# Kernel tuning notes

Hardware: AMD Instinct MI355X
Metric: run time of the kernel (lower is better)

## Reference

```python
import math
import jax, jax.numpy as jnp
import numpy as np

BS, NTOK, NHEADS, WIDTH, WIN = 2, 4096, 8, 32, 32


def _make_coo():
    d = np.repeat(np.arange(NTOK), WIN)
    j = np.tile(np.arange(WIN), NTOK)
    s = (d + j) % NTOK
    # dst_cnt = j (dense per-dst counter), src_cnt = j (dense per-src counter,
    # since for fixed src the contributing dsts have distinct j)
    return jnp.asarray(np.stack([d, s, j, j], axis=1), dtype=jnp.int32)


def setup_inputs() -> dict:
    key = jax.random.key(0)
    k1, k2, k3, k4 = jax.random.split(key, 4)
    shape = (BS, NTOK, NHEADS, WIDTH)
    return {
        "vf": jax.random.normal(k1, shape, dtype=jnp.float32),
        "vb": jax.random.normal(k2, shape, dtype=jnp.float32),
        "q": jax.random.normal(k3, shape, dtype=jnp.float32),
        "k": jax.random.normal(k4, shape, dtype=jnp.float32),
        "coo": _make_coo(),
        "dst_mxlen": WIN,
        "src_mxlen": WIN,
        "use_softmax": 1,
    }


def reference(vf, vb, q, k, coo, dst_mxlen, src_mxlen, use_softmax):
    # q,k,vf,vb: [bs, n_tok, n_heads, width]; coo: [cl,4] = [dst,src,dst_cnt,src_cnt]
    # COO formulation equivalent to the torch padded-dense buffers: padded slots
    # carry exp(-1e12)=0, sentinel column adds exp(0)=1 to each softmax denominator.
    dst, src = coo[:, 0], coo[:, 1]
    n_tok, width = q.shape[1], q.shape[3]
    scale = -1.0 / math.sqrt(width)
    # L1 attention scores per COO entry -> [cl, bs, h]
    ww = (jnp.sum(jnp.abs(q[:, dst] - k[:, src]), axis=-1) * scale).transpose(1, 0, 2)
    if use_softmax:
        # softmax per dst over its entries plus a zero sentinel slot
        m = jnp.maximum(jax.ops.segment_max(ww, dst, num_segments=n_tok), 0.0)  # [n_tok,bs,h]
        e = jnp.exp(ww - m[dst])
        denom = jax.ops.segment_sum(e, dst, num_segments=n_tok) + jnp.exp(-m)
        attn = e / denom[dst]  # [cl, bs, h]
    else:
        attn = jnp.exp(ww)
    # forward aggregation: per dst, weighted sum of vf[src]
    vfo = jax.ops.segment_sum(attn[..., None] * vf[:, src].transpose(1, 0, 2, 3),
                              dst, num_segments=n_tok)  # [n_tok, bs, h, w]
    # backward aggregation: per src, same weights applied to vb[dst]
    vbo = jax.ops.segment_sum(attn[..., None] * vb[:, dst].transpose(1, 0, 2, 3),
                              src, num_segments=n_tok)  # [n_tok, bs, h, w]
    return (vfo + vbo).transpose(1, 0, 2, 3)  # [bs, n_tok, h, w]
```

## Files before the change

kernel.cpp:

```cpp
#include <hip/hip_runtime.h>
#include <math.h>

#define BS 2
#define NTOK 4096
#define NMASK 4095
#define NHEADS 8
#define WIN 32
#define HALO 31
#define RA 95
#define RK 127
#define NTILES 64
#define SCALE (-0.17677669529663687f)

using u32 = unsigned int;
using h2 = __attribute__((ext_vector_type(2))) _Float16;
using h4 = __attribute__((ext_vector_type(4))) _Float16;
using f32x4 = __attribute__((ext_vector_type(4))) float;

static __device__ __forceinline__ u32 packrtz(float x, float y) {
  auto p = __builtin_amdgcn_cvt_pkrtz(x, y);
  return __builtin_bit_cast(u32, p);
}
static __device__ __forceinline__ h2 habs(h2 v) {
  return __builtin_bit_cast(h2, __builtin_bit_cast(u32, v) & 0x7fff7fffu);
}
static __device__ __forceinline__ float dot2acc(h2 a, float acc) {
#if __has_builtin(__builtin_amdgcn_fdot2)
  const h2 one = {(_Float16)1.f, (_Float16)1.f};
  return __builtin_amdgcn_fdot2(a, one, acc, false);
#else
  return acc + (float)a[0] + (float)a[1];
#endif
}

template <int CTRL>
static __device__ __forceinline__ float dppadd(float v) {
  int y = __builtin_amdgcn_update_dpp(0, __builtin_bit_cast(int, v), CTRL,
                                      0xF, 0xF, true);
  return v + __builtin_bit_cast(float, y);
}
static __device__ __forceinline__ float sum32(float v) {
  v = dppadd<0xB1>(v);
  v = dppadd<0x4E>(v);
  v = dppadd<0x141>(v);
  v = dppadd<0x140>(v);
  v += __shfl_xor(v, 16, 32);
  return v;
}

__global__ __launch_bounds__(256) void l1attn_fused(
    const float* __restrict__ q, const float* __restrict__ k,
    const float* __restrict__ vf, const float* __restrict__ vb,
    float* __restrict__ out, const int* __restrict__ use_sm_p) {
  const int tid = threadIdx.x;
  const int g = blockIdx.x;
  const int tile = g & (NTILES - 1);
  const int bh = g >> 6;
  const int h = bh & (NHEADS - 1);
  const int b = bh >> 3;
  const int t0 = tile << 6;

  const size_t base4 = ((size_t)b * NTOK) * 64 + (size_t)h * 8;
  const float4* qg = (const float4*)q;
  const float4* kg = (const float4*)k;
  const float4* vfg = (const float4*)vf;
  const float4* vbg = (const float4*)vb;

  __shared__ uint4 k_s[4 * 128];
  __shared__ uint4 q_s[4 * 96];
  __shared__ u32 vf_c[32 * 52];
  __shared__ u32 vb_c[32 * 52];
  __shared__ __align__(8) _Float16 atf[64 * 48];
  __shared__ __align__(8) _Float16 atb[64 * 52];

  for (int i = tid; i < RK * 4; i += 256) {
    int r = i >> 2, m = i & 3;
    int t = (t0 - HALO + r) & NMASK;
    const float4* krp = kg + base4 + (size_t)t * 64 + 2 * m;
    float4 v0 = krp[0], v1 = krp[1];
    k_s[m * 128 + r] = make_uint4(packrtz(v0.x, v0.y), packrtz(v0.z, v0.w),
                                  packrtz(v1.x, v1.y), packrtz(v1.z, v1.w));
  }
  for (int i = tid; i < 96 * 4; i += 256) {
    int r = i >> 2, m = i & 3;
    int t = (t0 - HALO + r) & NMASK;
    const float4* qrp = qg + base4 + (size_t)t * 64 + 2 * m;
    float4 v0 = qrp[0], v1 = qrp[1];
    q_s[m * 96 + r] = make_uint4(packrtz(v0.x, v0.y), packrtz(v0.z, v0.w),
                                 packrtz(v1.x, v1.y), packrtz(v1.z, v1.w));
  }
  for (int i = tid; i < 48 * 8; i += 256) {
    int rp = i >> 3, c = i & 7;
    int ta0 = (t0 + 2 * rp) & NMASK, ta1 = (t0 + 2 * rp + 1) & NMASK;
    float4 f0 = vfg[base4 + (size_t)ta0 * 64 + c];
    float4 f1 = vfg[base4 + (size_t)ta1 * 64 + c];
    vf_c[(4 * c + 0) * 52 + rp] = packrtz(f0.x, f1.x);
    vf_c[(4 * c + 1) * 52 + rp] = packrtz(f0.y, f1.y);
    vf_c[(4 * c + 2) * 52 + rp] = packrtz(f0.z, f1.z);
    vf_c[(4 * c + 3) * 52 + rp] = packrtz(f0.w, f1.w);
    int tb0 = (t0 - HALO + 2 * rp) & NMASK;
    int tb1 = (t0 - HALO + 2 * rp + 1) & NMASK;
    float4 g0 = vbg[base4 + (size_t)tb0 * 64 + c];
    float4 g1 = vbg[base4 + (size_t)tb1 * 64 + c];
    vb_c[(4 * c + 0) * 52 + rp] = packrtz(g0.x, g1.x);
    vb_c[(4 * c + 1) * 52 + rp] = packrtz(g0.y, g1.y);
    vb_c[(4 * c + 2) * 52 + rp] = packrtz(g0.z, g1.z);
    vb_c[(4 * c + 3) * 52 + rp] = packrtz(g0.w, g1.w);
  }
  {
    u32* az = (u32*)atf;
    for (int i = tid; i < 1536; i += 256) az[i] = 0;
    u32* bz = (u32*)atb;
    for (int i = tid; i < 1664; i += 256) bz[i] = 0;
  }
  __syncthreads();

  {
    const int lane = tid & 63, wid = tid >> 6;
    const int hh = lane >> 5, j = lane & 31;
    const int use_sm = *use_sm_p;
    const int row0 = wid * 24 + hh;

#pragma unroll
    for (int it = 0; it < 12; ++it) {
      const int row = row0 + it * 2;
      if (row < RA) {
        const int kr = row + j;
        float acc = 0.f;
#pragma unroll
        for (int m = 0; m < 4; ++m) {
          uint4 qq = q_s[m * 96 + row];
          uint4 kk = k_s[m * 128 + kr];
          acc = dot2acc(habs(__builtin_bit_cast(h2, qq.x) -
                             __builtin_bit_cast(h2, kk.x)), acc);
          acc = dot2acc(habs(__builtin_bit_cast(h2, qq.y) -
                             __builtin_bit_cast(h2, kk.y)), acc);
          acc = dot2acc(habs(__builtin_bit_cast(h2, qq.z) -
                             __builtin_bit_cast(h2, kk.z)), acc);
          acc = dot2acc(habs(__builtin_bit_cast(h2, qq.w) -
                             __builtin_bit_cast(h2, kk.w)), acc);
        }
        float e = __expf(acc * SCALE);
        float att;
        if (use_sm) {
          float s = sum32(e);
          att = e * __builtin_amdgcn_rcpf(1.f + s);
        } else {
          att = e;
        }
        _Float16 a16 = (_Float16)att;
        if (row >= HALO) {
          int tl = row - HALO;
          atf[tl * 48 + (tl & 15) + j] = a16;
        }
        int tl2 = row + j - HALO;
        if ((unsigned)tl2 < 64u) {
          atb[tl2 * 52 + (tl2 & 15) + 31 - j] = a16;
        }
      }
    }
  }
  __syncthreads();

  {
    const int l = tid & 63, wid = tid >> 6;
    const int r16 = l & 15, k4 = l >> 4;
    const _Float16* vfh = (const _Float16*)vf_c;
    const _Float16* vbh = (const _Float16*)vb_c;

    h4 afr[3], abr[3];
#pragma unroll
    for (int kt = 0; kt < 3; ++kt) {
      afr[kt] = *(const h4*)(atf + (wid * 16 + r16) * 48 + 16 * kt + 4 * k4);
      abr[kt] = *(const h4*)(atb + (wid * 16 + r16) * 52 + 16 * kt + 4 * k4);
    }
    const int kbase = 16 * wid + 4 * k4;
#pragma unroll
    for (int nt = 0; nt < 2; ++nt) {
      const int col = nt * 16 + r16;
      f32x4 acc = {0.f, 0.f, 0.f, 0.f};
#if __has_builtin(__builtin_amdgcn_mfma_f32_16x16x16f16)
#pragma unroll
      for (int kt = 0; kt < 3; ++kt) {
        h4 bf = *(const h4*)(vfh + col * 104 + kbase + 16 * kt);
        acc = __builtin_amdgcn_mfma_f32_16x16x16f16(afr[kt], bf, acc, 0, 0, 0);
      }
#pragma unroll
      for (int kt = 0; kt < 3; ++kt) {
        h4 bb = *(const h4*)(vbh + col * 104 + kbase + 16 * kt);
        acc = __builtin_amdgcn_mfma_f32_16x16x16f16(abr[kt], bb, acc, 0, 0, 0);
      }
#else
#pragma unroll
      for (int reg = 0; reg < 4; ++reg) {
        float s = 0.f;
        int mrow = 4 * k4 + reg;
        for (int kk = 0; kk < 48; ++kk) {
          s += (float)atf[(wid * 16 + mrow) * 48 + kk] *
                   (float)vfh[col * 104 + 16 * wid + kk] +
               (float)atb[(wid * 16 + mrow) * 52 + kk] *
                   (float)vbh[col * 104 + 16 * wid + kk];
        }
        acc[reg] = s;
      }
#endif
      const int t = t0 + 16 * wid + 4 * k4;
      const size_t ob =
          ((size_t)b * NTOK) * 256 + (size_t)t * 256 + h * 32 + col;
      out[ob] = acc[0];
      out[ob + 256] = acc[1];
      out[ob + 512] = acc[2];
      out[ob + 768] = acc[3];
    }
  }
}

extern "C" void kernel_launch(void* const* d_in, const int* in_sizes, int n_in,
                              void* d_out, int out_size, void* d_ws,
                              size_t ws_size, hipStream_t stream) {
  const float* vf = (const float*)d_in[0];
  const float* vb = (const float*)d_in[1];
  const float* q = (const float*)d_in[2];
  const float* k = (const float*)d_in[3];
  const int* use_sm = (const int*)d_in[7];
  float* out = (float*)d_out;

  const int blocks = BS * NHEADS * NTILES;
  l1attn_fused<<<blocks, 256, 0, stream>>>(q, k, vf, vb, out, use_sm);
}
```

Baseline: 24.63 us.

## Issue all global loads up front and defer vf/vb smem stores past scoring

The staging loops become straight-line code in which every thread issues all of its q, k, vf and vb global loads at once before any shared-memory store, so more loads are in flight together. The vf/vb values are held in registers across the score/softmax phase and written to shared memory only just before the second barrier, overlapping their memory latency with the L1-score compute. This raises register pressure (about 16 extra float4 live across the score loop), which may reduce occupancy.

```diff
diff --git a/kernel.cpp b/kernel.cpp
--- a/kernel.cpp
+++ b/kernel.cpp
@@ -20,6 +20,10 @@
 static __device__ __forceinline__ u32 packrtz(float x, float y) {
   auto p = __builtin_amdgcn_cvt_pkrtz(x, y);
   return __builtin_bit_cast(u32, p);
+}
+static __device__ __forceinline__ uint4 pack8(float4 a, float4 b) {
+  return make_uint4(packrtz(a.x, a.y), packrtz(a.z, a.w), packrtz(b.x, b.y),
+                    packrtz(b.z, b.w));
 }
 static __device__ __forceinline__ h2 habs(h2 v) {
   return __builtin_bit_cast(h2, __builtin_bit_cast(u32, v) & 0x7fff7fffu);
@@ -73,40 +77,51 @@
   __shared__ __align__(8) _Float16 atf[64 * 48];
   __shared__ __align__(8) _Float16 atb[64 * 52];
 
-  for (int i = tid; i < RK * 4; i += 256) {
-    int r = i >> 2, m = i & 3;
-    int t = (t0 - HALO + r) & NMASK;
-    const float4* krp = kg + base4 + (size_t)t * 64 + 2 * m;
-    float4 v0 = krp[0], v1 = krp[1];
-    k_s[m * 128 + r] = make_uint4(packrtz(v0.x, v0.y), packrtz(v0.z, v0.w),
-                                  packrtz(v1.x, v1.y), packrtz(v1.z, v1.w));
-  }
-  for (int i = tid; i < 96 * 4; i += 256) {
-    int r = i >> 2, m = i & 3;
-    int t = (t0 - HALO + r) & NMASK;
-    const float4* qrp = qg + base4 + (size_t)t * 64 + 2 * m;
-    float4 v0 = qrp[0], v1 = qrp[1];
-    q_s[m * 96 + r] = make_uint4(packrtz(v0.x, v0.y), packrtz(v0.z, v0.w),
-                                 packrtz(v1.x, v1.y), packrtz(v1.z, v1.w));
-  }
-  for (int i = tid; i < 48 * 8; i += 256) {
-    int rp = i >> 3, c = i & 7;
-    int ta0 = (t0 + 2 * rp) & NMASK, ta1 = (t0 + 2 * rp + 1) & NMASK;
-    float4 f0 = vfg[base4 + (size_t)ta0 * 64 + c];
-    float4 f1 = vfg[base4 + (size_t)ta1 * 64 + c];
-    vf_c[(4 * c + 0) * 52 + rp] = packrtz(f0.x, f1.x);
-    vf_c[(4 * c + 1) * 52 + rp] = packrtz(f0.y, f1.y);
-    vf_c[(4 * c + 2) * 52 + rp] = packrtz(f0.z, f1.z);
-    vf_c[(4 * c + 3) * 52 + rp] = packrtz(f0.w, f1.w);
-    int tb0 = (t0 - HALO + 2 * rp) & NMASK;
-    int tb1 = (t0 - HALO + 2 * rp + 1) & NMASK;
-    float4 g0 = vbg[base4 + (size_t)tb0 * 64 + c];
-    float4 g1 = vbg[base4 + (size_t)tb1 * 64 + c];
-    vb_c[(4 * c + 0) * 52 + rp] = packrtz(g0.x, g1.x);
-    vb_c[(4 * c + 1) * 52 + rp] = packrtz(g0.y, g1.y);
-    vb_c[(4 * c + 2) * 52 + rp] = packrtz(g0.z, g1.z);
-    vb_c[(4 * c + 3) * 52 + rp] = packrtz(g0.w, g1.w);
-  }
+  const int kr0 = tid >> 2, km0 = tid & 3;
+  const float4* kp0 =
+      kg + base4 + (size_t)((t0 - HALO + kr0) & NMASK) * 64 + 2 * km0;
+  float4 ka0 = kp0[0], ka1 = kp0[1];
+  const bool has_k1 = tid < RK * 4 - 256;
+  const int kr1 = (tid + 256) >> 2, km1 = (tid + 256) & 3;
+  float4 kb0, kb1;
+  if (has_k1) {
+    const float4* kp1 =
+        kg + base4 + (size_t)((t0 - HALO + kr1) & NMASK) * 64 + 2 * km1;
+    kb0 = kp1[0];
+    kb1 = kp1[1];
+  }
+  const int qr0 = tid >> 2, qm0 = tid & 3;
+  const float4* qp0 =
+      qg + base4 + (size_t)((t0 - HALO + qr0) & NMASK) * 64 + 2 * qm0;
+  float4 qa0 = qp0[0], qa1 = qp0[1];
+  const bool has_q1 = tid < 128;
+  const int qr1 = (tid + 256) >> 2, qm1 = (tid + 256) & 3;
+  float4 qb0, qb1;
+  if (has_q1) {
+    const float4* qp1 =
+        qg + base4 + (size_t)((t0 - HALO + qr1) & NMASK) * 64 + 2 * qm1;
+    qb0 = qp1[0];
+    qb1 = qp1[1];
+  }
+  const int rp0 = tid >> 3, c0 = tid & 7;
+  float4 f00 = vfg[base4 + (size_t)((t0 + 2 * rp0) & NMASK) * 64 + c0];
+  float4 f01 = vfg[base4 + (size_t)((t0 + 2 * rp0 + 1) & NMASK) * 64 + c0];
+  float4 g00 = vbg[base4 + (size_t)((t0 - HALO + 2 * rp0) & NMASK) * 64 + c0];
+  float4 g01 =
+      vbg[base4 + (size_t)((t0 - HALO + 2 * rp0 + 1) & NMASK) * 64 + c0];
+  const int rp1 = (tid + 256) >> 3, c1 = (tid + 256) & 7;
+  float4 f10, f11, g10, g11;
+  if (has_q1) {
+    f10 = vfg[base4 + (size_t)((t0 + 2 * rp1) & NMASK) * 64 + c1];
+    f11 = vfg[base4 + (size_t)((t0 + 2 * rp1 + 1) & NMASK) * 64 + c1];
+    g10 = vbg[base4 + (size_t)((t0 - HALO + 2 * rp1) & NMASK) * 64 + c1];
+    g11 = vbg[base4 + (size_t)((t0 - HALO + 2 * rp1 + 1) & NMASK) * 64 + c1];
+  }
+
+  k_s[km0 * 128 + kr0] = pack8(ka0, ka1);
+  if (has_k1) k_s[km1 * 128 + kr1] = pack8(kb0, kb1);
+  q_s[qm0 * 96 + qr0] = pack8(qa0, qa1);
+  if (has_q1) q_s[qm1 * 96 + qr1] = pack8(qb0, qb1);
   {
     u32* az = (u32*)atf;
     for (int i = tid; i < 1536; i += 256) az[i] = 0;
@@ -160,6 +175,25 @@
       }
     }
   }
+
+  vf_c[(4 * c0 + 0) * 52 + rp0] = packrtz(f00.x, f01.x);
+  vf_c[(4 * c0 + 1) * 52 + rp0] = packrtz(f00.y, f01.y);
+  vf_c[(4 * c0 + 2) * 52 + rp0] = packrtz(f00.z, f01.z);
+  vf_c[(4 * c0 + 3) * 52 + rp0] = packrtz(f00.w, f01.w);
+  vb_c[(4 * c0 + 0) * 52 + rp0] = packrtz(g00.x, g01.x);
+  vb_c[(4 * c0 + 1) * 52 + rp0] = packrtz(g00.y, g01.y);
+  vb_c[(4 * c0 + 2) * 52 + rp0] = packrtz(g00.z, g01.z);
+  vb_c[(4 * c0 + 3) * 52 + rp0] = packrtz(g00.w, g01.w);
+  if (has_q1) {
+    vf_c[(4 * c1 + 0) * 52 + rp1] = packrtz(f10.x, f11.x);
+    vf_c[(4 * c1 + 1) * 52 + rp1] = packrtz(f10.y, f11.y);
+    vf_c[(4 * c1 + 2) * 52 + rp1] = packrtz(f10.z, f11.z);
+    vf_c[(4 * c1 + 3) * 52 + rp1] = packrtz(f10.w, f11.w);
+    vb_c[(4 * c1 + 0) * 52 + rp1] = packrtz(g10.x, g11.x);
+    vb_c[(4 * c1 + 1) * 52 + rp1] = packrtz(g10.y, g11.y);
+    vb_c[(4 * c1 + 2) * 52 + rp1] = packrtz(g10.z, g11.z);
+    vb_c[(4 * c1 + 3) * 52 + rp1] = packrtz(g10.w, g11.w);
+  }
   __syncthreads();
 
   {
```

Result: faster. 22.12 us (-10.2%).
